# Kernel optimization log

Measured on AMD Instinct MI355X. Metric: run time of the kernel, lower is better.

## Reference

```python
import jax, jax.numpy as jnp
import numpy as np

NEG = -1e30  # log-space 'zero' (safe substitute for -inf)
EPS = 1e-7   # keras.backend.epsilon(), used by ctc_batch_cost


def _ctc_forward(logp, z, allow2):
    """CTC negative log-likelihood via the forward DP in log space.
    logp:   [B, T, C] log-probabilities
    z:      [B, S] extended label sequence (blanks interleaved), S = 2L+1
    allow2: [B, S] bool, whether the skip transition (s-2 -> s) is legal
    Returns [B, 1] loss (matches keras ctc_batch_cost output shape).
    """
    B, T, C = logp.shape
    S = z.shape[1]
    # Gather per-timestep log-probs of extended labels: [B, T, S] -> [T, B, S]
    b_idx = jnp.arange(B)[:, None, None]
    t_idx = jnp.arange(T)[None, :, None]
    lp_z = jnp.transpose(logp[b_idx, t_idx, z[:, None, :]], (1, 0, 2))

    s_idx = jnp.arange(S)[None, :]
    alpha0 = jnp.where(s_idx < 2, lp_z[0], NEG)  # paths may start at blank or first label

    def step(alpha, lp_t):
        a1 = jnp.concatenate([jnp.full((B, 1), NEG, alpha.dtype), alpha[:, :-1]], axis=1)
        a2 = jnp.concatenate([jnp.full((B, 2), NEG, alpha.dtype), alpha[:, :-2]], axis=1)
        a2 = jnp.where(allow2, a2, NEG)
        m = jnp.maximum(alpha, jnp.maximum(a1, a2))
        lse = m + jnp.log(jnp.exp(alpha - m) + jnp.exp(a1 - m) + jnp.exp(a2 - m))
        return lp_t + lse, None

    alphaT, _ = jax.lax.scan(step, alpha0, lp_z[1:])
    # Paths end at last blank (S-1) or last label (S-2)
    last, last2 = alphaT[:, -1], alphaT[:, -2]
    m = jnp.maximum(last, last2)
    ll = m + jnp.log(jnp.exp(last - m) + jnp.exp(last2 - m))
    return -ll[:, None]


def setup_inputs() -> dict:
    key = jax.random.key(0)
    k1, k2 = jax.random.split(key)
    B, T, C, L = 32, 2048, 256, 256
    # ctc_batch_cost expects post-softmax probabilities
    y_pred = jax.nn.softmax(jax.random.normal(k1, (B, T, C), jnp.float32), axis=-1)
    y_true = jax.random.randint(k2, (B, L), 0, C - 1)  # blank = C-1 excluded from labels
    return {"y_true": y_true, "y_pred": y_pred}


def reference(y_true, y_pred):
    B, T, C = y_pred.shape
    blank = C - 1
    L = y_true.shape[1]
    S = 2 * L + 1
    labels = y_true.astype(jnp.int32)
    # Extended label sequence: blank, l0, blank, l1, ..., blank
    z = jnp.full((B, S), blank, jnp.int32).at[:, 1::2].set(labels)
    z_m2 = jnp.concatenate([jnp.full((B, 2), -1, jnp.int32), z[:, :-2]], axis=1)
    allow2 = (z != blank) & (z != z_m2)
    logp = jnp.log(y_pred + EPS)
    return _ctc_forward(logp, z, allow2)
```

## Files before the change

kernel.cpp:

```cpp
#include <hip/hip_runtime.h>

#define TT   2048
#define CC   256
#define LL   256
#define SS   513
#define TM   1023
#define EPSF (1e-7f)
#define LN2F (0.69314718055994531f)
#define DPTH 8
#define RBTH 64
#define NCH  127
#define EMINI (-2000000000)
#define GSTR 260

#if __has_builtin(__builtin_amdgcn_frexp_expf)
#define FREXP_EXP __builtin_amdgcn_frexp_expf
#else
static __device__ __forceinline__ int FREXP_EXP(float x){ int e; return (frexpf(x,&e), e); }
#endif
#if __has_builtin(__builtin_amdgcn_ldexpf)
#define LDEXP __builtin_amdgcn_ldexpf
#else
#define LDEXP ldexpf
#endif

__launch_bounds__(256, 4)
__global__ void ctc_gather_kernel(const int* __restrict__ y_true,
                                  const float* __restrict__ y_pred,
                                  float* __restrict__ gat)
{
    const int b   = blockIdx.x;
    const int i   = threadIdx.x;
    const int col = y_true[b * LL + i];
    const float* rp = y_pred + (size_t)b * TT * CC;
    float*       gp = gat    + (size_t)b * TT * GSTR;
    const int tch = TT / gridDim.y;
    const int t0  = blockIdx.y * tch;
    #pragma unroll 4
    for (int t = t0; t < t0 + tch; ++t) {
        gp[(size_t)t * GSTR + i] = rp[(size_t)t * CC + col] + EPSF;
        if (i == 255)
            gp[(size_t)t * GSTR + 256] = rp[(size_t)t * CC + (CC - 1)] + EPSF;
    }
}

__launch_bounds__(128, 1)
__global__ void ctc_fast_kernel(const int* __restrict__ y_true,
                                const float* __restrict__ y_pred,
                                const float* __restrict__ gat,
                                float* __restrict__ out)
{
    __shared__ float cw[SS];
    __shared__ int   ew[64];

    const int tid   = threadIdx.x;
    const int w     = tid >> 6;
    const int lane  = tid & 63;
    const int b     = blockIdx.x;
    const int blank = CC - 1;

    const int*   lab   = y_true + b * LL;
    const float* base  = y_pred + (size_t)b * TT * CC;
    const float* gbase = gat    + (size_t)b * TT * GSTR;

    int   col0 = lab[4 * lane];
    float kup[4];
    float kdn[4];
    #pragma unroll
    for (int i = 0; i < 4; ++i) {
        const int li = 4 * lane + i;
        const int z  = lab[li];
        const int zm = (li >= 1) ? lab[li - 1] : -1;
        kup[i] = (z != zm) ? 1.0f : 0.0f;
        kdn[i] = (li <= 254 && lab[li + 1] != z) ? 1.0f : 0.0f;
    }

    float f[9];
    #pragma unroll
    for (int j = 0; j < 9; ++j) f[j] = 0.0f;
    int  e = 0;
    bool lzero;

    if (w == 0) {
        if (lane == 0) {
            f[0] = base[blank] + EPSF;
            f[1] = base[col0]  + EPSF;
        }
        lzero = (lane != 0);
    } else {
        if (lane == 63) {
            const float* rT = base + (size_t)(TT - 1) * CC;
            f[7] = rT[lab[255]] + EPSF;
            f[8] = rT[blank]    + EPSF;
        }
        lzero = (lane != 63);
    }

    float4 pf[DPTH];
    float  pbf[DPTH];
    #pragma unroll
    for (int k = 0; k < DPTH; ++k) {
        const int r = (w == 0) ? (1 + k) : (TT - 2 - k);
        const float* rp = gbase + (size_t)r * GSTR;
        pf[k]  = *(const float4*)(rp + 4 * lane);
        pbf[k] = rp[256];
    }

    auto renorm = [&]() {
        float m = fmaxf(fmaxf(fmaxf(f[0], f[1]), fmaxf(f[2], f[3])),
                        fmaxf(fmaxf(f[4], f[5]), fmaxf(f[6], fmaxf(f[7], f[8]))));
        const int em = FREXP_EXP(m);
        #pragma unroll
        for (int j = 0; j < 9; ++j) f[j] = LDEXP(f[j], -em);
        e += em;
    };

    auto fwd_step = [&](float pb, float p0, float p1, float p2, float p3) {
        float u7 = __shfl_up(f[7], 1);
        int   ue = __shfl_up(e, 1);
        if (lane == 0) { u7 = 0.0f; ue = e; }
        int dlt = ue - e;
        const bool rb = lzero || (dlt >= RBTH);
        if (__ballot(rb)) {
            const int sh = rb ? -dlt : 0;
            #pragma unroll
            for (int j = 0; j < 9; ++j) f[j] = LDEXP(f[j], sh);
            e   = rb ? ue : e;
            dlt = rb ? 0  : dlt;
            lzero = lzero && (u7 == 0.0f);
        }
        const float bf = LDEXP(u7, dlt);
        const float n0 = (f[0] + bf) * pb;
        const float n1 = (f[1] + f[0] + bf   * kup[0]) * p0;
        const float n2 = (f[2] + f[1]) * pb;
        const float n3 = (f[3] + f[2] + f[1] * kup[1]) * p1;
        const float n4 = (f[4] + f[3]) * pb;
        const float n5 = (f[5] + f[4] + f[3] * kup[2]) * p2;
        const float n6 = (f[6] + f[5]) * pb;
        const float n7 = (f[7] + f[6] + f[5] * kup[3]) * p3;
        const float n8 = (f[8] + f[7]) * pb;
        f[0]=n0; f[1]=n1; f[2]=n2; f[3]=n3; f[4]=n4;
        f[5]=n5; f[6]=n6; f[7]=n7; f[8]=n8;
    };

    auto bwd_step = [&](float pb, float p0, float p1, float p2, float p3) {
        float d1 = __shfl_down(f[1], 1);
        int   de = __shfl_down(e, 1);
        if (lane == 63) { d1 = 0.0f; de = e; }
        int dlt = de - e;
        const bool rb = lzero || (dlt >= RBTH);
        if (__ballot(rb)) {
            const int sh = rb ? -dlt : 0;
            #pragma unroll
            for (int j = 0; j < 9; ++j) f[j] = LDEXP(f[j], sh);
            e   = rb ? de : e;
            dlt = rb ? 0  : dlt;
            lzero = lzero && (d1 == 0.0f);
        }
        const float bf = LDEXP(d1, dlt);
        const float n0 = (f[0] + f[1]) * pb;
        const float n1 = (f[1] + f[2] + f[3] * kdn[0]) * p0;
        const float n2 = (f[2] + f[3]) * pb;
        const float n3 = (f[3] + f[4] + f[5] * kdn[1]) * p1;
        const float n4 = (f[4] + f[5]) * pb;
        const float n5 = (f[5] + f[6] + f[7] * kdn[2]) * p2;
        const float n6 = (f[6] + f[7]) * pb;
        const float n7 = (f[7] + f[8] + bf   * kdn[3]) * p3;
        const float n8 = (f[8] + bf) * pb;
        f[0]=n0; f[1]=n1; f[2]=n2; f[3]=n3; f[4]=n4;
        f[5]=n5; f[6]=n6; f[7]=n7; f[8]=n8;
    };

    if (w == 0) {
        for (int c = 0; c < NCH; ++c) {
            #pragma unroll
            for (int k = 0; k < DPTH; ++k) {
                const float pb = pbf[k];
                const float p0 = pf[k].x, p1 = pf[k].y,
                            p2 = pf[k].z, p3 = pf[k].w;
                int tp = 1 + c * DPTH + k + DPTH; if (tp > TM) tp = TM;
                const float* rp = gbase + (size_t)tp * GSTR;
                pf[k]  = *(const float4*)(rp + 4 * lane);
                pbf[k] = rp[256];
                fwd_step(pb, p0, p1, p2, p3);
                if (k == 3 || k == 7) renorm();
            }
        }
        #pragma unroll
        for (int k = 0; k < 7; ++k) {
            fwd_step(pbf[k], pf[k].x, pf[k].y, pf[k].z, pf[k].w);
            if (k == 3) renorm();
        }
    } else {
        for (int c = 0; c < NCH; ++c) {
            #pragma unroll
            for (int k = 0; k < DPTH; ++k) {
                const float pb = pbf[k];
                const float p0 = pf[k].x, p1 = pf[k].y,
                            p2 = pf[k].z, p3 = pf[k].w;
                int tp = (TT - 2) - (c * DPTH + k) - DPTH;
                if (tp < TM + 1) tp = TM + 1;
                const float* rp = gbase + (size_t)tp * GSTR;
                pf[k]  = *(const float4*)(rp + 4 * lane);
                pbf[k] = rp[256];
                bwd_step(pb, p0, p1, p2, p3);
                if (k == 3 || k == 7) renorm();
            }
        }
        #pragma unroll
        for (int k = 0; k < 7; ++k) {
            bwd_step(pbf[k], pf[k].x, pf[k].y, pf[k].z, pf[k].w);
            if (k == 3) renorm();
        }

        float d1 = __shfl_down(f[1], 1);
        int   de = __shfl_down(e, 1);
        if (lane == 63) { d1 = 0.0f; de = e; }
        int dlt = de - e;
        if (dlt >= RBTH) {
            #pragma unroll
            for (int j = 0; j < 9; ++j) f[j] = LDEXP(f[j], -dlt);
            e = de; dlt = 0;
        }
        const float bf = LDEXP(d1, dlt);
        float cb[9];
        cb[0] = f[0] + f[1];
        cb[1] = f[1] + f[2] + f[3] * kdn[0];
        cb[2] = f[2] + f[3];
        cb[3] = f[3] + f[4] + f[5] * kdn[1];
        cb[4] = f[4] + f[5];
        cb[5] = f[5] + f[6] + f[7] * kdn[2];
        cb[6] = f[6] + f[7];
        cb[7] = f[7] + f[8] + bf   * kdn[3];
        cb[8] = f[8] + bf;

        #pragma unroll
        for (int j = 0; j < 8; ++j) cw[8 * lane + j] = cb[j];
        if (lane == 63) cw[512] = cb[8];
        ew[lane] = e;
    }

    __syncthreads();

    if (w == 0) {
        float part = 0.0f;
        #pragma unroll
        for (int j = 0; j < 8; ++j) part += f[j] * cw[8 * lane + j];
        if (lane == 63) part += f[8] * cw[512];
        int   ep = (part > 0.0f) ? (e + ew[lane]) : EMINI;
        float m  = part;
        #pragma unroll
        for (int d = 1; d < 64; d <<= 1) {
            const float mo = __shfl_xor(m, d);
            const int   eo = __shfl_xor(ep, d);
            const int   E  = ep > eo ? ep : eo;
            m  = LDEXP(m, ep - E) + LDEXP(mo, eo - E);
            ep = E;
        }
        if (lane == 0)
            out[b] = -LN2F * ((float)ep + __builtin_amdgcn_logf(m));
    }
}

__launch_bounds__(128, 1)
__global__ void ctc_fb_kernel(const int* __restrict__ y_true,
                              const float* __restrict__ y_pred,
                              float* __restrict__ out)
{
    __shared__ float cw[SS];
    __shared__ int   ew[64];

    const int tid   = threadIdx.x;
    const int w     = tid >> 6;
    const int lane  = tid & 63;
    const int b     = blockIdx.x;
    const int blank = CC - 1;

    const int*   lab  = y_true + b * LL;
    const float* base = y_pred + (size_t)b * TT * CC;

    int   col[4];
    float kup[4], kdn[4];
    #pragma unroll
    for (int i = 0; i < 4; ++i) {
        const int li = 4 * lane + i;
        const int z  = lab[li];
        col[i] = z;
        const int zm = (li >= 1) ? lab[li - 1] : -1;
        kup[i] = (z != zm) ? 1.0f : 0.0f;
        kdn[i] = (li <= 254 && lab[li + 1] != z) ? 1.0f : 0.0f;
    }

    float f[9];
    #pragma unroll
    for (int j = 0; j < 9; ++j) f[j] = 0.0f;
    int  e = 0;
    bool lzero;

    if (w == 0) {
        if (lane == 0) { f[0] = base[blank] + EPSF; f[1] = base[col[0]] + EPSF; }
        lzero = (lane != 0);
    } else {
        if (lane == 63) {
            const float* rT = base + (size_t)(TT - 1) * CC;
            f[7] = rT[col[3]] + EPSF; f[8] = rT[blank] + EPSF;
        }
        lzero = (lane != 63);
    }

    float pfb[DPTH]; float pfl[DPTH][4];
    #pragma unroll
    for (int k = 0; k < DPTH; ++k) {
        const int r = (w == 0) ? (1 + k) : (TT - 2 - k);
        const float* rp = base + (size_t)r * CC;
        pfb[k] = rp[blank];
        #pragma unroll
        for (int i = 0; i < 4; ++i) pfl[k][i] = rp[col[i]];
    }

    auto renorm = [&]() {
        float m = fmaxf(fmaxf(fmaxf(f[0], f[1]), fmaxf(f[2], f[3])),
                        fmaxf(fmaxf(f[4], f[5]), fmaxf(f[6], fmaxf(f[7], f[8]))));
        const int em = FREXP_EXP(m);
        #pragma unroll
        for (int j = 0; j < 9; ++j) f[j] = LDEXP(f[j], -em);
        e += em;
    };
    auto fwd_step = [&](float pb, float p0, float p1, float p2, float p3) {
        float u7 = __shfl_up(f[7], 1);
        int   ue = __shfl_up(e, 1);
        if (lane == 0) { u7 = 0.0f; ue = e; }
        int dlt = ue - e;
        const bool rb = lzero || (dlt >= RBTH);
        if (__ballot(rb)) {
            const int sh = rb ? -dlt : 0;
            #pragma unroll
            for (int j = 0; j < 9; ++j) f[j] = LDEXP(f[j], sh);
            e = rb ? ue : e; dlt = rb ? 0 : dlt;
            lzero = lzero && (u7 == 0.0f);
        }
        const float bf = LDEXP(u7, dlt);
        const float n0 = (f[0] + bf) * pb;
        const float n1 = (f[1] + f[0] + bf   * kup[0]) * p0;
        const float n2 = (f[2] + f[1]) * pb;
        const float n3 = (f[3] + f[2] + f[1] * kup[1]) * p1;
        const float n4 = (f[4] + f[3]) * pb;
        const float n5 = (f[5] + f[4] + f[3] * kup[2]) * p2;
        const float n6 = (f[6] + f[5]) * pb;
        const float n7 = (f[7] + f[6] + f[5] * kup[3]) * p3;
        const float n8 = (f[8] + f[7]) * pb;
        f[0]=n0; f[1]=n1; f[2]=n2; f[3]=n3; f[4]=n4;
        f[5]=n5; f[6]=n6; f[7]=n7; f[8]=n8;
    };
    auto bwd_step = [&](float pb, float p0, float p1, float p2, float p3) {
        float d1 = __shfl_down(f[1], 1);
        int   de = __shfl_down(e, 1);
        if (lane == 63) { d1 = 0.0f; de = e; }
        int dlt = de - e;
        const bool rb = lzero || (dlt >= RBTH);
        if (__ballot(rb)) {
            const int sh = rb ? -dlt : 0;
            #pragma unroll
            for (int j = 0; j < 9; ++j) f[j] = LDEXP(f[j], sh);
            e = rb ? de : e; dlt = rb ? 0 : dlt;
            lzero = lzero && (d1 == 0.0f);
        }
        const float bf = LDEXP(d1, dlt);
        const float n0 = (f[0] + f[1]) * pb;
        const float n1 = (f[1] + f[2] + f[3] * kdn[0]) * p0;
        const float n2 = (f[2] + f[3]) * pb;
        const float n3 = (f[3] + f[4] + f[5] * kdn[1]) * p1;
        const float n4 = (f[4] + f[5]) * pb;
        const float n5 = (f[5] + f[6] + f[7] * kdn[2]) * p2;
        const float n6 = (f[6] + f[7]) * pb;
        const float n7 = (f[7] + f[8] + bf   * kdn[3]) * p3;
        const float n8 = (f[8] + bf) * pb;
        f[0]=n0; f[1]=n1; f[2]=n2; f[3]=n3; f[4]=n4;
        f[5]=n5; f[6]=n6; f[7]=n7; f[8]=n8;
    };

    if (w == 0) {
        for (int c = 0; c < NCH; ++c) {
            #pragma unroll
            for (int k = 0; k < DPTH; ++k) {
                const float pb = pfb[k] + EPSF;
                const float p0 = pfl[k][0] + EPSF, p1 = pfl[k][1] + EPSF;
                const float p2 = pfl[k][2] + EPSF, p3 = pfl[k][3] + EPSF;
                int tp = 1 + c * DPTH + k + DPTH; if (tp > TM) tp = TM;
                const float* rp = base + (size_t)tp * CC;
                pfb[k] = rp[blank];
                #pragma unroll
                for (int i = 0; i < 4; ++i) pfl[k][i] = rp[col[i]];
                fwd_step(pb, p0, p1, p2, p3);
                if (k == 3 || k == 7) renorm();
            }
        }
        #pragma unroll
        for (int k = 0; k < 7; ++k) {
            fwd_step(pfb[k] + EPSF, pfl[k][0] + EPSF, pfl[k][1] + EPSF,
                     pfl[k][2] + EPSF, pfl[k][3] + EPSF);
            if (k == 3) renorm();
        }
    } else {
        for (int c = 0; c < NCH; ++c) {
            #pragma unroll
            for (int k = 0; k < DPTH; ++k) {
                const float pb = pfb[k] + EPSF;
                const float p0 = pfl[k][0] + EPSF, p1 = pfl[k][1] + EPSF;
                const float p2 = pfl[k][2] + EPSF, p3 = pfl[k][3] + EPSF;
                int tp = (TT - 2) - (c * DPTH + k) - DPTH; if (tp < TM + 1) tp = TM + 1;
                const float* rp = base + (size_t)tp * CC;
                pfb[k] = rp[blank];
                #pragma unroll
                for (int i = 0; i < 4; ++i) pfl[k][i] = rp[col[i]];
                bwd_step(pb, p0, p1, p2, p3);
                if (k == 3 || k == 7) renorm();
            }
        }
        #pragma unroll
        for (int k = 0; k < 7; ++k) {
            bwd_step(pfb[k] + EPSF, pfl[k][0] + EPSF, pfl[k][1] + EPSF,
                     pfl[k][2] + EPSF, pfl[k][3] + EPSF);
            if (k == 3) renorm();
        }

        float d1 = __shfl_down(f[1], 1);
        int   de = __shfl_down(e, 1);
        if (lane == 63) { d1 = 0.0f; de = e; }
        int dlt = de - e;
        if (dlt >= RBTH) {
            #pragma unroll
            for (int j = 0; j < 9; ++j) f[j] = LDEXP(f[j], -dlt);
            e = de; dlt = 0;
        }
        const float bf = LDEXP(d1, dlt);
        float cb[9];
        cb[0] = f[0] + f[1];
        cb[1] = f[1] + f[2] + f[3] * kdn[0];
        cb[2] = f[2] + f[3];
        cb[3] = f[3] + f[4] + f[5] * kdn[1];
        cb[4] = f[4] + f[5];
        cb[5] = f[5] + f[6] + f[7] * kdn[2];
        cb[6] = f[6] + f[7];
        cb[7] = f[7] + f[8] + bf   * kdn[3];
        cb[8] = f[8] + bf;
        #pragma unroll
        for (int j = 0; j < 8; ++j) cw[8 * lane + j] = cb[j];
        if (lane == 63) cw[512] = cb[8];
        ew[lane] = e;
    }

    __syncthreads();

    if (w == 0) {
        float part = 0.0f;
        #pragma unroll
        for (int j = 0; j < 8; ++j) part += f[j] * cw[8 * lane + j];
        if (lane == 63) part += f[8] * cw[512];
        int   ep = (part > 0.0f) ? (e + ew[lane]) : EMINI;
        float m  = part;
        #pragma unroll
        for (int d = 1; d < 64; d <<= 1) {
            const float mo = __shfl_xor(m, d);
            const int   eo = __shfl_xor(ep, d);
            const int   E  = ep > eo ? ep : eo;
            m  = LDEXP(m, ep - E) + LDEXP(mo, eo - E);
            ep = E;
        }
        if (lane == 0)
            out[b] = -LN2F * ((float)ep + __builtin_amdgcn_logf(m));
    }
}

extern "C" void kernel_launch(void* const* d_in, const int* in_sizes, int n_in,
                              void* d_out, int out_size, void* d_ws, size_t ws_size,
                              hipStream_t stream)
{
    const int*   y_true = (const int*)d_in[0];
    const float* y_pred = (const float*)d_in[1];
    float*       out    = (float*)d_out;
    const int B = in_sizes[0] / LL;

    const size_t need = (size_t)B * TT * GSTR * sizeof(float);
    if (ws_size >= need) {
        float* gat = (float*)d_ws;
        ctc_gather_kernel<<<dim3(B, 32), 256, 0, stream>>>(y_true, y_pred, gat);
        ctc_fast_kernel<<<B, 128, 0, stream>>>(y_true, y_pred, gat, out);
    } else {
        ctc_fb_kernel<<<B, 128, 0, stream>>>(y_true, y_pred, out);
    }
}
```

Before: 205.1 us.

## Stage gathered rows into LDS ring via async global_load_lds and split blank array

The gathered workspace is split into a dense 256-wide label-probability array and a separate per-timestep blank array. The DP kernel no longer keeps an 8-deep register prefetch. It streams rows into an 8-slot LDS ring with global_load_lds and paces the loads with explicit vmcnt waits, and it stages the whole blank column into LDS once up front. This is meant to cut register pressure and hide global load latency in the serial recurrence, at the cost of extra LDS usage and a per-step LDS read and wait.

```diff
diff --git a/kernel.cpp b/kernel.cpp
--- a/kernel.cpp
+++ b/kernel.cpp
@@ -11,7 +11,7 @@
 #define RBTH 64
 #define NCH  127
 #define EMINI (-2000000000)
-#define GSTR 260
+#define GL   256
 
 #if __has_builtin(__builtin_amdgcn_frexp_expf)
 #define FREXP_EXP __builtin_amdgcn_frexp_expf
@@ -24,32 +24,50 @@
 #define LDEXP ldexpf
 #endif
 
+__device__ __forceinline__ void stage16(const float* g, float* l)
+{
+    __builtin_amdgcn_global_load_lds(
+        (const __attribute__((address_space(1))) unsigned int*)g,
+        (__attribute__((address_space(3))) unsigned int*)l,
+        16, 0, 0);
+}
+
+#define VMWAIT(N) do {                                        \
+        asm volatile("s_waitcnt vmcnt(" #N ")" ::: "memory"); \
+        __builtin_amdgcn_sched_barrier(0);                    \
+    } while (0)
+
 __launch_bounds__(256, 4)
 __global__ void ctc_gather_kernel(const int* __restrict__ y_true,
                                   const float* __restrict__ y_pred,
-                                  float* __restrict__ gat)
+                                  float* __restrict__ gatL,
+                                  float* __restrict__ blankA)
 {
     const int b   = blockIdx.x;
     const int i   = threadIdx.x;
     const int col = y_true[b * LL + i];
     const float* rp = y_pred + (size_t)b * TT * CC;
-    float*       gp = gat    + (size_t)b * TT * GSTR;
+    float*       gp = gatL   + (size_t)b * TT * GL;
+    float*       bp = blankA + (size_t)b * TT;
     const int tch = TT / gridDim.y;
     const int t0  = blockIdx.y * tch;
     #pragma unroll 4
     for (int t = t0; t < t0 + tch; ++t) {
-        gp[(size_t)t * GSTR + i] = rp[(size_t)t * CC + col] + EPSF;
+        gp[(size_t)t * GL + i] = rp[(size_t)t * CC + col] + EPSF;
         if (i == 255)
-            gp[(size_t)t * GSTR + 256] = rp[(size_t)t * CC + (CC - 1)] + EPSF;
+            bp[t] = rp[(size_t)t * CC + (CC - 1)] + EPSF;
     }
 }
 
 __launch_bounds__(128, 1)
 __global__ void ctc_fast_kernel(const int* __restrict__ y_true,
                                 const float* __restrict__ y_pred,
-                                const float* __restrict__ gat,
+                                const float* __restrict__ gatL,
+                                const float* __restrict__ blankA,
                                 float* __restrict__ out)
 {
+    __shared__ __align__(16) float ring[2][8][GL];
+    __shared__ __align__(16) float blk[2][TT];
     __shared__ float cw[SS];
     __shared__ int   ew[64];
 
@@ -61,11 +79,12 @@
 
     const int*   lab   = y_true + b * LL;
     const float* base  = y_pred + (size_t)b * TT * CC;
-    const float* gbase = gat    + (size_t)b * TT * GSTR;
-
-    int   col0 = lab[4 * lane];
+    const float* gLb   = gatL   + (size_t)b * TT * GL;
+    const float* bAb   = blankA + (size_t)b * TT;
+
     float kup[4];
     float kdn[4];
+    const int col0 = lab[4 * lane];
     #pragma unroll
     for (int i = 0; i < 4; ++i) {
         const int li = 4 * lane + i;
@@ -94,16 +113,6 @@
             f[8] = rT[blank]    + EPSF;
         }
         lzero = (lane != 63);
-    }
-
-    float4 pf[DPTH];
-    float  pbf[DPTH];
-    #pragma unroll
-    for (int k = 0; k < DPTH; ++k) {
-        const int r = (w == 0) ? (1 + k) : (TT - 2 - k);
-        const float* rp = gbase + (size_t)r * GSTR;
-        pf[k]  = *(const float4*)(rp + 4 * lane);
-        pbf[k] = rp[256];
     }
 
     auto renorm = [&]() {
@@ -171,46 +180,56 @@
         f[5]=n5; f[6]=n6; f[7]=n7; f[8]=n8;
     };
 
+    {
+        const float* bsrc = bAb + 4 * lane;
+        #pragma unroll
+        for (int ch = 0; ch < 8; ++ch)
+            stage16(bsrc + ch * 256, &blk[w][ch * 256]);
+        #pragma unroll
+        for (int k = 0; k < 8; ++k) {
+            const int r = w ? (2046 - k) : (1 + k);
+            stage16(gLb + (size_t)r * GL + 4 * lane, &ring[w][k][0]);
+        }
+    }
+    VMWAIT(7);
+    float4 nx4 = *(const float4*)&ring[w][0][4 * lane];
+    float  nxb = blk[w][w ? 2046 : 1];
+
     if (w == 0) {
-        for (int c = 0; c < NCH; ++c) {
-            #pragma unroll
-            for (int k = 0; k < DPTH; ++k) {
-                const float pb = pbf[k];
-                const float p0 = pf[k].x, p1 = pf[k].y,
-                            p2 = pf[k].z, p3 = pf[k].w;
-                int tp = 1 + c * DPTH + k + DPTH; if (tp > TM) tp = TM;
-                const float* rp = gbase + (size_t)tp * GSTR;
-                pf[k]  = *(const float4*)(rp + 4 * lane);
-                pbf[k] = rp[256];
-                fwd_step(pb, p0, p1, p2, p3);
-                if (k == 3 || k == 7) renorm();
+        const float* gs = gLb + (size_t)9 * GL + 4 * lane;
+        int rowN = 2;
+        for (int i = 0; i < 1023; ++i) {
+            const float4 c4 = nx4; const float cb = nxb;
+            fwd_step(cb, c4.x, c4.y, c4.z, c4.w);
+            if ((i & 3) == 3) renorm();
+            if (i <= 1014) { VMWAIT(6); } else { VMWAIT(0); }
+            if (i < 1022) {
+                nx4 = *(const float4*)&ring[0][(i + 1) & 7][4 * lane];
+                nxb = blk[0][rowN];
+                ++rowN;
             }
-        }
-        #pragma unroll
-        for (int k = 0; k < 7; ++k) {
-            fwd_step(pbf[k], pf[k].x, pf[k].y, pf[k].z, pf[k].w);
-            if (k == 3) renorm();
+            if (i <= 1014) {
+                stage16(gs, &ring[0][i & 7][0]);
+                gs += GL;
+            }
         }
     } else {
-        for (int c = 0; c < NCH; ++c) {
-            #pragma unroll
-            for (int k = 0; k < DPTH; ++k) {
-                const float pb = pbf[k];
-                const float p0 = pf[k].x, p1 = pf[k].y,
-                            p2 = pf[k].z, p3 = pf[k].w;
-                int tp = (TT - 2) - (c * DPTH + k) - DPTH;
-                if (tp < TM + 1) tp = TM + 1;
-                const float* rp = gbase + (size_t)tp * GSTR;
-                pf[k]  = *(const float4*)(rp + 4 * lane);
-                pbf[k] = rp[256];
-                bwd_step(pb, p0, p1, p2, p3);
-                if (k == 3 || k == 7) renorm();
+        const float* gs = gLb + (size_t)2038 * GL + 4 * lane;
+        int rowN = 2045;
+        for (int i = 0; i < 1023; ++i) {
+            const float4 c4 = nx4; const float cb = nxb;
+            bwd_step(cb, c4.x, c4.y, c4.z, c4.w);
+            if ((i & 3) == 3) renorm();
+            if (i <= 1014) { VMWAIT(6); } else { VMWAIT(0); }
+            if (i < 1022) {
+                nx4 = *(const float4*)&ring[1][(i + 1) & 7][4 * lane];
+                nxb = blk[1][rowN];
+                --rowN;
             }
-        }
-        #pragma unroll
-        for (int k = 0; k < 7; ++k) {
-            bwd_step(pbf[k], pf[k].x, pf[k].y, pf[k].z, pf[k].w);
-            if (k == 3) renorm();
+            if (i <= 1014) {
+                stage16(gs, &ring[1][i & 7][0]);
+                gs -= GL;
+            }
         }
 
         float d1 = __shfl_down(f[1], 1);
@@ -481,11 +500,13 @@
     float*       out    = (float*)d_out;
     const int B = in_sizes[0] / LL;
 
-    const size_t need = (size_t)B * TT * GSTR * sizeof(float);
+    const size_t gatl_elems = (size_t)B * TT * GL;
+    const size_t need = (gatl_elems + (size_t)B * TT) * sizeof(float);
     if (ws_size >= need) {
-        float* gat = (float*)d_ws;
-        ctc_gather_kernel<<<dim3(B, 32), 256, 0, stream>>>(y_true, y_pred, gat);
-        ctc_fast_kernel<<<B, 128, 0, stream>>>(y_true, y_pred, gat, out);
+        float* gatL   = (float*)d_ws;
+        float* blankA = gatL + gatl_elems;
+        ctc_gather_kernel<<<dim3(B, 32), 256, 0, stream>>>(y_true, y_pred, gatL, blankA);
+        ctc_fast_kernel<<<B, 128, 0, stream>>>(y_true, y_pred, gatL, blankA, out);
     } else {
         ctc_fb_kernel<<<B, 128, 0, stream>>>(y_true, y_pred, out);
     }
```

Result: slower. 318.2 us (+55.2%).
